# Kernel optimization log

Measured on AMD Instinct MI355X. Metric: run time of the kernel, lower is better.

## Reference

```python
import jax, jax.numpy as jnp
import numpy as np

D_MODEL = 1024
N_HEADS = 16
D_Q = 64
D_V = 64
N_SEG = 16
EPS_LN = 1e-5
EPS_MEM = 1e-6


def setup_inputs() -> dict:
    key = jax.random.key(0)
    ks = jax.random.split(key, 10)
    N, T = 4, 4096
    inp = {
        "query_sequences": jax.random.normal(ks[0], (N, T, D_MODEL), dtype=jnp.float32),
        "key_sequences": jax.random.normal(ks[1], (N, T, D_MODEL), dtype=jnp.float32),
        "value_sequences": jax.random.normal(ks[2], (N, T, D_MODEL), dtype=jnp.float32),
        "Wq": jax.random.normal(ks[3], (D_MODEL, N_HEADS * D_Q), dtype=jnp.float32) * 0.02,
        "Wk": jax.random.normal(ks[4], (D_MODEL, N_HEADS * D_Q), dtype=jnp.float32) * 0.02,
        "Wv": jax.random.normal(ks[5], (D_MODEL, N_HEADS * D_V), dtype=jnp.float32) * 0.02,
        "Wo": jax.random.normal(ks[6], (N_HEADS * D_V, D_MODEL), dtype=jnp.float32) * 0.02,
        "ln_w": jnp.ones((D_MODEL,), dtype=jnp.float32),
        "ln_b": jnp.zeros((D_MODEL,), dtype=jnp.float32),
        "beta": jnp.ones((1,), dtype=jnp.float32),
    }
    return inp


def _layer_norm(x, w, b):
    mu = jnp.mean(x, axis=-1, keepdims=True)
    var = jnp.var(x, axis=-1, keepdims=True)
    return (x - mu) * jax.lax.rsqrt(var + EPS_LN) * w + b


def reference(query_sequences, key_sequences, value_sequences, Wq, Wk, Wv, Wo, ln_w, ln_b, beta):
    N, t, _ = query_sequences.shape
    S = t // N_SEG  # segment length (256)

    # qkv_norm applied to q, and (self-attention) to k and v as well
    qn = _layer_norm(query_sequences, ln_w, ln_b)
    kn = _layer_norm(key_sequences, ln_w, ln_b)
    vn = _layer_norm(value_sequences, ln_w, ln_b)

    # project and split heads -> [N, H, t, d]
    qh = (qn @ Wq).reshape(N, t, N_HEADS, D_Q).transpose(0, 2, 1, 3)
    kh = (kn @ Wk).reshape(N, t, N_HEADS, D_Q).transpose(0, 2, 1, 3)
    vh = (vn @ Wv).reshape(N, t, N_HEADS, D_V).transpose(0, 2, 1, 3)

    # segment: [N_SEG, N, H, S, d] so lax.scan iterates segments sequentially
    seg = lambda x, d: x.reshape(N, N_HEADS, N_SEG, S, d).transpose(2, 0, 1, 3, 4)
    q_segs, k_segs, v_segs = seg(qh, D_Q), seg(kh, D_Q), seg(vh, D_V)

    b_gate = jax.nn.sigmoid(beta)[0]            # scalar mixing gate
    scale = 1.0 / np.sqrt(D_Q).astype(np.float32)
    causal = jnp.tril(jnp.ones((S, S), dtype=bool))

    def step(carry, xs):
        mem, z = carry                          # [N,H,Dq,Dv], [N,H,Dq]
        qs, ks_, vs = xs                        # [N,H,S,d]
        sq = jax.nn.elu(qs) + 1.0
        sk = jax.nn.elu(ks_) + 1.0
        # retrieve from compressive memory
        num = jnp.einsum('nhsd,nhde->nhse', sq, mem)
        den = jnp.einsum('nhsd,nhd->nhs', sq, z)[..., None] + EPS_MEM
        a_mem = num / den                       # [N,H,S,Dv]
        # local causal softmax attention within the segment
        scores = jnp.einsum('nhsd,nhtd->nhst', qs, ks_) * scale
        scores = jnp.where(causal, scores, -jnp.inf)
        probs = jax.nn.softmax(scores, axis=-1)
        attn = jnp.einsum('nhst,nhtd->nhsd', probs, vs)
        out = b_gate * a_mem + (1.0 - b_gate) * attn
        # linear memory update
        mem = mem + jnp.einsum('nhsd,nhse->nhde', sk, vs)
        z = z + sk.sum(axis=2)
        return (mem, z), out

    mem0 = jnp.zeros((N, N_HEADS, D_Q, D_V), dtype=query_sequences.dtype)
    z0 = jnp.zeros((N, N_HEADS, D_Q), dtype=query_sequences.dtype)
    _, outs = jax.lax.scan(step, (mem0, z0), (q_segs, k_segs, v_segs))

    # outs: [N_SEG, N, H, S, Dv] -> [N, t, H*Dv]
    seqs = outs.transpose(1, 0, 3, 2, 4).reshape(N, t, N_HEADS * D_V)
    return seqs @ Wo
```

## Files before the change

kernel.cpp:

```cpp
#include <hip/hip_runtime.h>
#include <stdint.h>
#include <math.h>


typedef __attribute__((ext_vector_type(8))) short bf16x8_t;
typedef __attribute__((ext_vector_type(4))) short short4_t;
typedef __attribute__((ext_vector_type(4))) float f32x4;

__device__ __forceinline__ float bf2f(short s){
  union { unsigned u; float f; } v; v.u = ((unsigned)(unsigned short)s) << 16; return v.f;
}
__device__ __forceinline__ short f2bf(float f){
  union { float fl; unsigned u; } v; v.fl = f;
  unsigned r = v.u + 0x7FFFu + ((v.u >> 16) & 1u);
  return (short)(unsigned short)(r >> 16);
}
__device__ __forceinline__ f32x4 mfma16(bf16x8_t a, bf16x8_t b, f32x4 c){
  return __builtin_amdgcn_mfma_f32_16x16x32_bf16(a, b, c, 0, 0, 0);
}
__device__ __forceinline__ void gl_lds16(const short* g, short* l){
  __builtin_amdgcn_global_load_lds((const __attribute__((address_space(1))) void*)g,
                                   (__attribute__((address_space(3))) void*)l, 16, 0, 0);
}

__global__ __launch_bounds__(256) void ln3(const float* __restrict__ xq, const float* __restrict__ xk,
                                           const float* __restrict__ xv,
                                           const float* __restrict__ gw, const float* __restrict__ gb,
                                           short* __restrict__ oq, short* __restrict__ ok,
                                           short* __restrict__ ov){
  const int row = blockIdx.x, which = blockIdx.y, tid = threadIdx.x;
  const float* x = which == 0 ? xq : which == 1 ? xk : xv;
  short* out     = which == 0 ? oq : which == 1 ? ok : ov;
  const float4 v = *reinterpret_cast<const float4*>(x + (size_t)row*1024 + tid*4);
  float s  = v.x + v.y + v.z + v.w;
  float s2 = v.x*v.x + v.y*v.y + v.z*v.z + v.w*v.w;
  #pragma unroll
  for (int off = 1; off < 64; off <<= 1){
    s  += __shfl_xor(s,  off);
    s2 += __shfl_xor(s2, off);
  }
  __shared__ float red[8];
  if ((tid & 63) == 0){ red[tid>>6] = s; red[4 + (tid>>6)] = s2; }
  __syncthreads();
  s  = red[0] + red[1] + red[2] + red[3];
  s2 = red[4] + red[5] + red[6] + red[7];
  const float mu  = s * (1.0f/1024.0f);
  const float var = s2 * (1.0f/1024.0f) - mu*mu;
  const float rs  = rsqrtf(var + 1e-5f);
  const float4 wv = *reinterpret_cast<const float4*>(gw + tid*4);
  const float4 bv = *reinterpret_cast<const float4*>(gb + tid*4);
  short4_t o;
  o[0] = f2bf((v.x-mu)*rs*wv.x + bv.x);
  o[1] = f2bf((v.y-mu)*rs*wv.y + bv.y);
  o[2] = f2bf((v.z-mu)*rs*wv.z + bv.z);
  o[3] = f2bf((v.w-mu)*rs*wv.w + bv.w);
  *reinterpret_cast<short4_t*>(out + (size_t)row*1024 + tid*4) = o;
}

__global__ __launch_bounds__(256) void wcast4(const float* __restrict__ W0, const float* __restrict__ W1,
                                              const float* __restrict__ W2, const float* __restrict__ W3,
                                              short* __restrict__ T0, short* __restrict__ T1,
                                              short* __restrict__ T2, short* __restrict__ T3){
  const int z = blockIdx.z;
  const float* W = z == 0 ? W0 : z == 1 ? W1 : z == 2 ? W2 : W3;
  short* Wt      = z == 0 ? T0 : z == 1 ? T1 : z == 2 ? T2 : T3;
  __shared__ float tile[64][65];
  const int bx = blockIdx.x, by = blockIdx.y, tid = threadIdx.x;
  #pragma unroll
  for (int p=0;p<4;++p){
    int idx = p*256 + tid;
    int r = idx >> 4, c4 = (idx & 15) << 2;
    const float4 v = *reinterpret_cast<const float4*>(W + (size_t)(by*64 + r)*1024 + bx*64 + c4);
    tile[r][c4+0] = v.x; tile[r][c4+1] = v.y; tile[r][c4+2] = v.z; tile[r][c4+3] = v.w;
  }
  __syncthreads();
  #pragma unroll
  for (int p=0;p<4;++p){
    int idx = p*256 + tid;
    int r = idx >> 4, c4 = (idx & 15) << 2;
    short4_t o;
    o[0] = f2bf(tile[c4+0][r]); o[1] = f2bf(tile[c4+1][r]);
    o[2] = f2bf(tile[c4+2][r]); o[3] = f2bf(tile[c4+3][r]);
    *reinterpret_cast<short4_t*>(Wt + (size_t)(bx*64 + r)*1024 + by*64 + c4) = o;
  }
}

__device__ __forceinline__ void remap_mc(int n, int& m0, int& c0){
  int xcd = n & 7, idx = n >> 3;
  m0 = ((xcd << 3) + (idx & 7)) << 8;
  c0 = (idx >> 3) << 8;
}

__device__ __forceinline__ void gemm_body(short* smem, const short* __restrict__ A,
                                          const short* __restrict__ Bt, void* __restrict__ C,
                                          int mode, int m0, int c0){
  short* As = smem;
  short* Bs = smem + 32768;
  const int tid = threadIdx.x;
  const int lane = tid & 63, wid = tid >> 6;
  const int wr = wid >> 2, wc = wid & 3;
  const int l15 = lane & 15, lhi = lane >> 4;

  const short* Asrc[4]; const short* Bsrc[4];
  #pragma unroll
  for (int p=0;p<4;++p){
    int i = tid + 512*p;
    int r = i >> 3, g = (i & 7) ^ (r & 7);
    Asrc[p] = A  + (size_t)(m0 + r)*1024 + g*8;
    Bsrc[p] = Bt + (size_t)(c0 + r)*1024 + g*8;
  }

  f32x4 acc[8][4];
  #pragma unroll
  for (int m=0;m<8;++m)
    #pragma unroll
    for (int n=0;n<4;++n) acc[m][n] = (f32x4){0.f,0.f,0.f,0.f};

  #define STAGE_A(t) { short* _d=&As[((t)&1)<<14]; int _k=(t)<<6; \
      gl_lds16(Asrc[0]+_k, _d+tid*8); gl_lds16(Asrc[1]+_k, _d+4096+tid*8); \
      gl_lds16(Asrc[2]+_k, _d+8192+tid*8); gl_lds16(Asrc[3]+_k, _d+12288+tid*8); }
  #define STAGE_B(t) { short* _d=&Bs[((t)&1)<<14]; int _k=(t)<<6; \
      gl_lds16(Bsrc[0]+_k, _d+tid*8); gl_lds16(Bsrc[1]+_k, _d+4096+tid*8); \
      gl_lds16(Bsrc[2]+_k, _d+8192+tid*8); gl_lds16(Bsrc[3]+_k, _d+12288+tid*8); }

  STAGE_A(0); STAGE_B(0);
  asm volatile("s_waitcnt vmcnt(0)" ::: "memory");
  __builtin_amdgcn_s_barrier();

  for (int t = 0; t < 16; ++t){
    const short* Ab = &As[(t & 1) << 14];
    const short* Bb = &Bs[(t & 1) << 14];
    if (t < 15){ STAGE_A(t+1); STAGE_B(t+1); }
    bf16x8_t af[4][2], bfr[4][2];
    #pragma unroll
    for (int m=0;m<4;++m){
      int r = wr*128 + m*16 + l15;
      #pragma unroll
      for (int ks=0;ks<2;++ks){
        int sl = (ks*4 + lhi) ^ (r & 7);
        af[m][ks] = *reinterpret_cast<const bf16x8_t*>(&Ab[r*64 + sl*8]);
      }
    }
    #pragma unroll
    for (int n=0;n<2;++n){
      int r = wc*64 + n*16 + l15;
      #pragma unroll
      for (int ks=0;ks<2;++ks){
        int sl = (ks*4 + lhi) ^ (r & 7);
        bfr[n][ks] = *reinterpret_cast<const bf16x8_t*>(&Bb[r*64 + sl*8]);
      }
    }
    __builtin_amdgcn_s_setprio(1);
    #pragma unroll
    for (int m=0;m<4;++m)
      #pragma unroll
      for (int n=0;n<2;++n)
        #pragma unroll
        for (int ks=0;ks<2;++ks)
          acc[m][n] = mfma16(af[m][ks], bfr[n][ks], acc[m][n]);
    __builtin_amdgcn_s_setprio(0);
    #pragma unroll
    for (int n=2;n<4;++n){
      int r = wc*64 + n*16 + l15;
      #pragma unroll
      for (int ks=0;ks<2;++ks){
        int sl = (ks*4 + lhi) ^ (r & 7);
        bfr[n][ks] = *reinterpret_cast<const bf16x8_t*>(&Bb[r*64 + sl*8]);
      }
    }
    __builtin_amdgcn_s_setprio(1);
    #pragma unroll
    for (int m=0;m<4;++m)
      #pragma unroll
      for (int n=2;n<4;++n)
        #pragma unroll
        for (int ks=0;ks<2;++ks)
          acc[m][n] = mfma16(af[m][ks], bfr[n][ks], acc[m][n]);
    __builtin_amdgcn_s_setprio(0);
    #pragma unroll
    for (int m=0;m<4;++m){
      int r = wr*128 + 64 + m*16 + l15;
      #pragma unroll
      for (int ks=0;ks<2;++ks){
        int sl = (ks*4 + lhi) ^ (r & 7);
        af[m][ks] = *reinterpret_cast<const bf16x8_t*>(&Ab[r*64 + sl*8]);
      }
    }
    __builtin_amdgcn_s_setprio(1);
    #pragma unroll
    for (int m=0;m<4;++m)
      #pragma unroll
      for (int n=0;n<2;++n)
        #pragma unroll
        for (int ks=0;ks<2;++ks)
          acc[4+m][n] = mfma16(af[m][ks], bfr[n][ks], acc[4+m][n]);
    __builtin_amdgcn_s_setprio(0);
    __builtin_amdgcn_s_setprio(1);
    #pragma unroll
    for (int m=0;m<4;++m)
      #pragma unroll
      for (int n=2;n<4;++n)
        #pragma unroll
        for (int ks=0;ks<2;++ks)
          acc[4+m][n] = mfma16(af[m][ks], bfr[n][ks], acc[4+m][n]);
    __builtin_amdgcn_s_setprio(0);
    asm volatile("s_waitcnt vmcnt(0)" ::: "memory");
    __builtin_amdgcn_s_barrier();
  }
  #undef STAGE_A
  #undef STAGE_B

  if (mode == 0){
    short* Cb = (short*)C;
    #pragma unroll
    for (int m=0;m<8;++m)
      #pragma unroll
      for (int n=0;n<4;++n)
        #pragma unroll
        for (int j=0;j<4;++j){
          int row = m0 + wr*128 + m*16 + lhi*4 + j;
          int col = c0 + wc*64 + n*16 + l15;
          size_t oidx = ((size_t)((row>>12)*16 + (col>>6)) * 4096 + (size_t)(row & 4095)) * 64 + (col & 63);
          Cb[oidx] = f2bf(acc[m][n][j]);
        }
  } else if (mode == 2){
    short* Cb = (short*)C;
    #pragma unroll
    for (int m=0;m<8;++m)
      #pragma unroll
      for (int n=0;n<4;++n){
        int rowb = m0 + wr*128 + m*16 + lhi*4;
        int col  = c0 + wc*64 + n*16 + l15;
        int nh = ((rowb>>12)<<4) + (col>>6);
        int e  = col & 63;
        int tt = rowb & 4095;
        short4_t o;
        #pragma unroll
        for (int j=0;j<4;++j) o[j] = f2bf(acc[m][n][j]);
        *reinterpret_cast<short4_t*>(&Cb[((size_t)nh*64 + e)*4096 + tt]) = o;
      }
  } else {
    float* Cf = (float*)C;
    #pragma unroll
    for (int m=0;m<8;++m)
      #pragma unroll
      for (int n=0;n<4;++n)
        #pragma unroll
        for (int j=0;j<4;++j){
          int row = m0 + wr*128 + m*16 + lhi*4 + j;
          int col = c0 + wc*64 + n*16 + l15;
          Cf[(size_t)row*1024 + col] = acc[m][n][j];
        }
  }
}

__global__ __launch_bounds__(512, 2) void gemm_qkv(const short* __restrict__ A0, const short* __restrict__ A1,
    const short* __restrict__ A2, const short* __restrict__ B0, const short* __restrict__ B1,
    const short* __restrict__ B2, short* __restrict__ C0, short* __restrict__ C1, short* __restrict__ C2){
  extern __shared__ short smem[];
  const int z = blockIdx.z;
  const short* A = z == 0 ? A0 : z == 1 ? A1 : A2;
  const short* B = z == 0 ? B0 : z == 1 ? B1 : B2;
  short* C       = z == 0 ? C0 : z == 1 ? C1 : C2;
  int m0, c0; remap_mc(blockIdx.x + 64*blockIdx.y, m0, c0);
  gemm_body(smem, A, B, (void*)C, z == 2 ? 2 : 0, m0, c0);
}

__global__ __launch_bounds__(512, 2) void gemm_wo(const short* __restrict__ A, const short* __restrict__ Bt,
                                                  float* __restrict__ C){
  extern __shared__ short smem[];
  int m0, c0; remap_mc(blockIdx.x + 64*blockIdx.y, m0, c0);
  gemm_body(smem, A, Bt, (void*)C, 1, m0, c0);
}

__global__ __launch_bounds__(256) void stageA(const short* __restrict__ kh, const short* __restrict__ vhT,
                                              short* __restrict__ delta_b, float* __restrict__ zd){
  const int seg = blockIdx.x, nh = blockIdx.y, tid = threadIdx.x;
  const int lane = tid & 63, w = tid >> 6;
  const int l15 = lane & 15, lhi = lane >> 4;
  __shared__ short skT[64*256];
  const size_t thead = (size_t)nh*4096 + (size_t)seg*256;

  #pragma unroll
  for (int ch=0; ch<8; ++ch){
    int s  = ch*32 + (tid>>3);
    int lc = (tid&7)*8;
    bf16x8_t kv = *reinterpret_cast<const bf16x8_t*>(kh + (thead + s)*64 + lc);
    #pragma unroll
    for (int j=0;j<8;++j){
      float f = bf2f(kv[j]);
      short sv = f2bf((f > 0.f) ? (f + 1.f) : __expf(f));
      int d = lc + j;
      int bo = ((d*256 + s) << 1) ^ (((d>>3)&7) << 4);
      *reinterpret_cast<short*>(reinterpret_cast<char*>(skT) + bo) = sv;
    }
  }
  __syncthreads();

  bf16x8_t ones;
  #pragma unroll
  for (int i=0;i<8;++i) ones[i] = (short)0x3F80;

  f32x4 dacc[4], zacc[4];
  #pragma unroll
  for (int jf=0;jf<4;++jf){ dacc[jf] = (f32x4){0.f,0.f,0.f,0.f}; zacc[jf] = (f32x4){0.f,0.f,0.f,0.f}; }

  #pragma unroll
  for (int ks=0; ks<8; ++ks){
    bf16x8_t av = *reinterpret_cast<const bf16x8_t*>(
        vhT + ((size_t)nh*64 + w*16 + l15)*4096 + (size_t)seg*256 + ks*32 + lhi*8);
    #pragma unroll
    for (int jf=0;jf<4;++jf){
      int d  = jf*16 + l15;
      int so = ks*32 + lhi*8;
      int bo = ((d*256 + so) << 1) ^ (((d>>3)&7) << 4);
      bf16x8_t bk = *reinterpret_cast<const bf16x8_t*>(reinterpret_cast<char*>(skT) + bo);
      dacc[jf] = mfma16(av, bk, dacc[jf]);
      if (w == 0) zacc[jf] = mfma16(ones, bk, zacc[jf]);
    }
  }

  short* dp = delta_b + (size_t)(seg*64 + nh)*4096;
  #pragma unroll
  for (int jf=0;jf<4;++jf)
    #pragma unroll
    for (int j=0;j<4;++j)
      dp[(w*16 + lhi*4 + j)*64 + jf*16 + l15] = f2bf(dacc[jf][j]);
  if (w == 0 && lhi == 0){
    #pragma unroll
    for (int jf=0;jf<4;++jf)
      zd[(size_t)(seg*64 + nh)*64 + jf*16 + l15] = zacc[jf][0];
  }
}

__global__ __launch_bounds__(256) void stageB(const short* __restrict__ delta_b, const float* __restrict__ zd,
                                              short* __restrict__ mpre_b, float* __restrict__ zpre){
  const int c = blockIdx.x, nh = blockIdx.y, tid = threadIdx.x;
  const int idx = c*256 + tid;
  float acc = 0.f;
  for (int seg=0; seg<16; ++seg){
    size_t b = (size_t)(seg*64 + nh)*4096 + idx;
    mpre_b[b] = f2bf(acc);
    acc += bf2f(delta_b[b]);
  }
  if (c == 0 && tid < 64){
    float za = 0.f;
    for (int seg=0; seg<16; ++seg){
      size_t zb = (size_t)(seg*64 + nh)*64 + tid;
      zpre[zb] = za;
      za += zd[zb];
    }
  }
}

__global__ __launch_bounds__(256, 3) void stageC(const short* __restrict__ qh, const short* __restrict__ kh,
    const short* __restrict__ vhT, const short* __restrict__ mpre_b, const float* __restrict__ z_pre,
    const float* __restrict__ beta, short* __restrict__ seqs)
{
  const int seg  = blockIdx.x;
  const int nh   = blockIdx.y;
  const int tid = threadIdx.x;
  const int lane = tid & 63, w = tid >> 6;
  const int l15 = lane & 15, lhi = lane >> 4;

  __shared__ float zl[64];
  __shared__ short pl[4][32][72];

  const size_t thead = (size_t)nh*4096 + (size_t)seg*256;

  if (tid < 64) zl[tid] = z_pre[(size_t)(seg*64 + nh)*64 + tid];
  __syncthreads();

  const float bg = 1.f / (1.f + __expf(-beta[0]));
  const float scale = 0.125f;
  bf16x8_t ones;
  #pragma unroll
  for (int i=0;i<8;++i) ones[i] = (short)0x3F80;
  const short* mpbase = mpre_b + (size_t)(seg*64 + nh)*4096;
  const int nb = nh >> 4, hh = nh & 15;

  for (int p = 0; p < 2; ++p){
    const int tile = p ? (7 - w) : w;
    const int nkt  = (tile >> 1) + 1;
    const int rb   = tile * 32;

    bf16x8_t aq[2][2];
    #pragma unroll
    for (int m=0;m<2;++m)
      #pragma unroll
      for (int ks=0;ks<2;++ks)
        aq[m][ks] = *reinterpret_cast<const bf16x8_t*>(qh + (thead + rb + m*16 + l15)*64 + ks*32 + lhi*8);

    f32x4 o_acc[2][4], l_acc[2];
    #pragma unroll
    for (int m=0;m<2;++m){
      l_acc[m] = (f32x4){0.f,0.f,0.f,0.f};
      #pragma unroll
      for (int jf=0;jf<4;++jf) o_acc[m][jf] = (f32x4){0.f,0.f,0.f,0.f};
    }

    for (int kt = 0; kt < nkt; ++kt){
      bf16x8_t bv[4][2];
      #pragma unroll
      for (int jf=0;jf<4;++jf)
        #pragma unroll
        for (int ks2=0;ks2<2;++ks2)
          bv[jf][ks2] = *reinterpret_cast<const bf16x8_t*>(
              vhT + ((size_t)nh*64 + jf*16 + l15)*4096 + (size_t)seg*256 + kt*64 + ks2*32 + lhi*8);

      f32x4 s_acc[2][4];
      #pragma unroll
      for (int m=0;m<2;++m)
        #pragma unroll
        for (int jf=0;jf<4;++jf) s_acc[m][jf] = (f32x4){0.f,0.f,0.f,0.f};
      #pragma unroll
      for (int ks=0;ks<2;++ks){
        bf16x8_t bk[4];
        #pragma unroll
        for (int jf=0;jf<4;++jf)
          bk[jf] = *reinterpret_cast<const bf16x8_t*>(kh + (thead + kt*64 + jf*16 + l15)*64 + ks*32 + lhi*8);
        #pragma unroll
        for (int m=0;m<2;++m)
          #pragma unroll
          for (int jf=0;jf<4;++jf)
            s_acc[m][jf] = mfma16(aq[m][ks], bk[jf], s_acc[m][jf]);
      }
      const bool lastkt = (kt == nkt - 1);
      #pragma unroll
      for (int m=0;m<2;++m)
        #pragma unroll
        for (int jf=0;jf<4;++jf)
          #pragma unroll
          for (int j=0;j<4;++j){
            float vv = s_acc[m][jf][j] * scale;
            if (lastkt){
              int sr = rb + m*16 + lhi*4 + j;
              int tc = kt*64 + jf*16 + l15;
              if (tc > sr) vv = -INFINITY;
            }
            float pv = __expf(vv);
            pl[w][m*16 + lhi*4 + j][jf*16 + l15] = f2bf(pv);
          }
      #pragma unroll
      for (int ks2=0;ks2<2;++ks2){
        bf16x8_t ap[2];
        #pragma unroll
        for (int m=0;m<2;++m)
          ap[m] = *reinterpret_cast<const bf16x8_t*>(&pl[w][m*16 + l15][ks2*32 + lhi*8]);
        #pragma unroll
        for (int m=0;m<2;++m){
          l_acc[m] = mfma16(ap[m], ones, l_acc[m]);
          #pragma unroll
          for (int jf=0;jf<4;++jf)
            o_acc[m][jf] = mfma16(ap[m], bv[jf][ks2], o_acc[m][jf]);
        }
      }
    }

    bf16x8_t sq[2][2];
    #pragma unroll
    for (int m=0;m<2;++m)
      #pragma unroll
      for (int ks=0;ks<2;++ks)
        #pragma unroll
        for (int i=0;i<8;++i){
          float f = bf2f(aq[m][ks][i]);
          sq[m][ks][i] = f2bf((f > 0.f) ? (f + 1.f) : __expf(f));
        }
    bf16x8_t bz[2];
    #pragma unroll
    for (int ks=0;ks<2;++ks)
      #pragma unroll
      for (int i=0;i<8;++i) bz[ks][i] = f2bf(zl[ks*32 + lhi*8 + i]);

    f32x4 n_acc[2][4], d_acc[2];
    #pragma unroll
    for (int m=0;m<2;++m){
      d_acc[m] = (f32x4){0.f,0.f,0.f,0.f};
      #pragma unroll
      for (int jf=0;jf<4;++jf) n_acc[m][jf] = (f32x4){0.f,0.f,0.f,0.f};
    }
    #pragma unroll
    for (int ks=0;ks<2;++ks){
      bf16x8_t bm[4];
      #pragma unroll
      for (int jf=0;jf<4;++jf)
        bm[jf] = *reinterpret_cast<const bf16x8_t*>(mpbase + (jf*16 + l15)*64 + ks*32 + lhi*8);
      #pragma unroll
      for (int m=0;m<2;++m){
        #pragma unroll
        for (int jf=0;jf<4;++jf) n_acc[m][jf] = mfma16(sq[m][ks], bm[jf], n_acc[m][jf]);
        d_acc[m] = mfma16(sq[m][ks], bz[ks], d_acc[m]);
      }
    }

    #pragma unroll
    for (int m=0;m<2;++m)
      #pragma unroll
      for (int jf=0;jf<4;++jf)
        #pragma unroll
        for (int j=0;j<4;++j){
          float attn = o_acc[m][jf][j] / l_acc[m][j];
          float amem = n_acc[m][jf][j] / (d_acc[m][j] + 1e-6f);
          float ov = bg*amem + (1.f-bg)*attn;
          int srow = rb + m*16 + lhi*4 + j;
          seqs[((size_t)nb*4096 + (size_t)seg*256 + srow)*1024 + hh*64 + jf*16 + l15] = f2bf(ov);
        }
  }
}

extern "C" void kernel_launch(void* const* d_in, const int* in_sizes, int n_in,
                              void* d_out, int out_size, void* d_ws, size_t ws_size,
                              hipStream_t stream){
  (void)in_sizes; (void)n_in; (void)out_size; (void)ws_size;
  const float* q    = (const float*)d_in[0];
  const float* k    = (const float*)d_in[1];
  const float* v    = (const float*)d_in[2];
  const float* Wq   = (const float*)d_in[3];
  const float* Wk   = (const float*)d_in[4];
  const float* Wv   = (const float*)d_in[5];
  const float* Wo   = (const float*)d_in[6];
  const float* lnw  = (const float*)d_in[7];
  const float* lnb  = (const float*)d_in[8];
  const float* beta = (const float*)d_in[9];
  char* ws = (char*)d_ws;
  const size_t MB = 1024ull*1024ull;
  short* WqT    = (short*)(ws + 0*MB);
  short* WkT    = (short*)(ws + 2*MB);
  short* WvT    = (short*)(ws + 4*MB);
  short* WoT    = (short*)(ws + 6*MB);
  short* xn_v   = (short*)(ws + 8*MB);
  short* seqs   = xn_v;
  short* qh     = (short*)(ws + 40*MB);
  short* kh     = (short*)(ws + 72*MB);
  short* vhT    = (short*)(ws + 104*MB);
  short* delta_b= (short*)(ws + 136*MB);
  float* zd     = (float*)(ws + 144*MB);
  short* mpre_b = (short*)(ws + 145*MB);
  float* zpre   = (float*)(ws + 153*MB);
  short* xn_q   = (short*)d_out;
  short* xn_k   = (short*)d_out + 16384ull*1024ull;

  wcast4<<<dim3(16,16,4),256,0,stream>>>(Wq,Wk,Wv,Wo, WqT,WkT,WvT,WoT);
  ln3<<<dim3(16384,3),256,0,stream>>>(q,k,v, lnw,lnb, xn_q,xn_k,xn_v);

  const size_t lds_gemm = 131072;
  gemm_qkv<<<dim3(64,4,3),512,lds_gemm,stream>>>(xn_q,xn_k,xn_v, WqT,WkT,WvT, qh,kh,vhT);

  stageA<<<dim3(16,64),256,0,stream>>>(kh, vhT, delta_b, zd);
  stageB<<<dim3(16,64),256,0,stream>>>(delta_b, zd, mpre_b, zpre);
  stageC<<<dim3(16,64),256,0,stream>>>(qh, kh, vhT, mpre_b, zpre, beta, seqs);
  gemm_wo<<<dim3(64,4),512,lds_gemm,stream>>>(seqs, WoT, (float*)d_out);
}
```

Baseline: 314.9 us.

## Stage K/V tiles in LDS with double-buffering and give each wave 64 query rows

StageC now cooperatively loads 64-row K and V tiles into XOR-swizzled shared memory with global_load_lds, double-buffered across the four key tiles. Each wave now owns one 64-row query block instead of two 32-row tiles. Before, every wave re-read K and V from global memory on its own. The load-balancing pairing of tiles (w and 7-w) is gone, so waves do uneven causal work (1 to 4 key tiles), and there are more per-iteration barriers. Register use rises (4x4 accumulators) and the occupancy hint is dropped.

```diff
diff --git a/kernel.cpp b/kernel.cpp
--- a/kernel.cpp
+++ b/kernel.cpp
@@ -353,7 +353,7 @@
   }
 }
 
-__global__ __launch_bounds__(256, 3) void stageC(const short* __restrict__ qh, const short* __restrict__ kh,
+__global__ __launch_bounds__(256) void stageC(const short* __restrict__ qh, const short* __restrict__ kh,
     const short* __restrict__ vhT, const short* __restrict__ mpre_b, const float* __restrict__ z_pre,
     const float* __restrict__ beta, short* __restrict__ seqs)
 {
@@ -363,12 +363,37 @@
   const int lane = tid & 63, w = tid >> 6;
   const int l15 = lane & 15, lhi = lane >> 4;
 
+  __shared__ short Ks[2][4096];
+  __shared__ short Vs[2][4096];
   __shared__ float zl[64];
-  __shared__ short pl[4][32][72];
+  __shared__ short pl[4][64][72];
 
   const size_t thead = (size_t)nh*4096 + (size_t)seg*256;
 
+  const short* Ksrc[2]; const short* Vsrc[2];
+  #pragma unroll
+  for (int p=0;p<2;++p){
+    int i = tid + 256*p, r = i >> 3, g = (i & 7) ^ (r & 7);
+    Ksrc[p] = kh + (thead + r)*64 + g*8;
+    Vsrc[p] = vhT + ((size_t)nh*64 + r)*4096 + (size_t)seg*256 + g*8;
+  }
+  #define STAGE_KV(kt) { short* _kd = Ks[(kt)&1]; short* _vd = Vs[(kt)&1]; \
+      gl_lds16(Ksrc[0] + (kt)*4096, _kd + tid*8); \
+      gl_lds16(Ksrc[1] + (kt)*4096, _kd + 2048 + tid*8); \
+      gl_lds16(Vsrc[0] + (kt)*64,  _vd + tid*8); \
+      gl_lds16(Vsrc[1] + (kt)*64,  _vd + 2048 + tid*8); }
+
   if (tid < 64) zl[tid] = z_pre[(size_t)(seg*64 + nh)*64 + tid];
+
+  bf16x8_t aq[4][2];
+  #pragma unroll
+  for (int m=0;m<4;++m)
+    #pragma unroll
+    for (int ks=0;ks<2;++ks)
+      aq[m][ks] = *reinterpret_cast<const bf16x8_t*>(qh + (thead + w*64 + m*16 + l15)*64 + ks*32 + lhi*8);
+
+  STAGE_KV(0);
+  asm volatile("s_waitcnt vmcnt(0)" ::: "memory");
   __syncthreads();
 
   const float bg = 1.f / (1.f + __expf(-beta[0]));
@@ -376,66 +401,51 @@
   bf16x8_t ones;
   #pragma unroll
   for (int i=0;i<8;++i) ones[i] = (short)0x3F80;
-  const short* mpbase = mpre_b + (size_t)(seg*64 + nh)*4096;
-  const int nb = nh >> 4, hh = nh & 15;
-
-  for (int p = 0; p < 2; ++p){
-    const int tile = p ? (7 - w) : w;
-    const int nkt  = (tile >> 1) + 1;
-    const int rb   = tile * 32;
-
-    bf16x8_t aq[2][2];
-    #pragma unroll
-    for (int m=0;m<2;++m)
-      #pragma unroll
-      for (int ks=0;ks<2;++ks)
-        aq[m][ks] = *reinterpret_cast<const bf16x8_t*>(qh + (thead + rb + m*16 + l15)*64 + ks*32 + lhi*8);
-
-    f32x4 o_acc[2][4], l_acc[2];
-    #pragma unroll
-    for (int m=0;m<2;++m){
-      l_acc[m] = (f32x4){0.f,0.f,0.f,0.f};
-      #pragma unroll
-      for (int jf=0;jf<4;++jf) o_acc[m][jf] = (f32x4){0.f,0.f,0.f,0.f};
-    }
-
-    for (int kt = 0; kt < nkt; ++kt){
-      bf16x8_t bv[4][2];
-      #pragma unroll
-      for (int jf=0;jf<4;++jf)
-        #pragma unroll
-        for (int ks2=0;ks2<2;++ks2)
-          bv[jf][ks2] = *reinterpret_cast<const bf16x8_t*>(
-              vhT + ((size_t)nh*64 + jf*16 + l15)*4096 + (size_t)seg*256 + kt*64 + ks2*32 + lhi*8);
-
-      f32x4 s_acc[2][4];
-      #pragma unroll
-      for (int m=0;m<2;++m)
+
+  f32x4 o_acc[4][4], l_acc[4];
+  #pragma unroll
+  for (int m=0;m<4;++m){
+    l_acc[m] = (f32x4){0.f,0.f,0.f,0.f};
+    #pragma unroll
+    for (int jf=0;jf<4;++jf) o_acc[m][jf] = (f32x4){0.f,0.f,0.f,0.f};
+  }
+
+  for (int kt = 0; kt < 4; ++kt){
+    const short* Kb = Ks[kt & 1];
+    const short* Vb = Vs[kt & 1];
+    if (kt < 3) STAGE_KV(kt+1);
+    if (kt <= w){
+      f32x4 s_acc[4][4];
+      #pragma unroll
+      for (int m=0;m<4;++m)
         #pragma unroll
         for (int jf=0;jf<4;++jf) s_acc[m][jf] = (f32x4){0.f,0.f,0.f,0.f};
       #pragma unroll
       for (int ks=0;ks<2;++ks){
         bf16x8_t bk[4];
         #pragma unroll
-        for (int jf=0;jf<4;++jf)
-          bk[jf] = *reinterpret_cast<const bf16x8_t*>(kh + (thead + kt*64 + jf*16 + l15)*64 + ks*32 + lhi*8);
-        #pragma unroll
-        for (int m=0;m<2;++m)
+        for (int jf=0;jf<4;++jf){
+          int r = jf*16 + l15;
+          int sl = (ks*4 + lhi) ^ (r & 7);
+          bk[jf] = *reinterpret_cast<const bf16x8_t*>(&Kb[r*64 + sl*8]);
+        }
+        #pragma unroll
+        for (int m=0;m<4;++m)
           #pragma unroll
           for (int jf=0;jf<4;++jf)
             s_acc[m][jf] = mfma16(aq[m][ks], bk[jf], s_acc[m][jf]);
       }
-      const bool lastkt = (kt == nkt - 1);
-      #pragma unroll
-      for (int m=0;m<2;++m)
+      const bool diag = (kt == w);
+      #pragma unroll
+      for (int m=0;m<4;++m)
         #pragma unroll
         for (int jf=0;jf<4;++jf)
           #pragma unroll
           for (int j=0;j<4;++j){
             float vv = s_acc[m][jf][j] * scale;
-            if (lastkt){
-              int sr = rb + m*16 + lhi*4 + j;
-              int tc = kt*64 + jf*16 + l15;
+            if (diag){
+              int sr = (w<<6) + m*16 + lhi*4 + j;
+              int tc = (kt<<6) + jf*16 + l15;
               if (tc > sr) vv = -INFINITY;
             }
             float pv = __expf(vv);
@@ -443,70 +453,83 @@
           }
       #pragma unroll
       for (int ks2=0;ks2<2;++ks2){
-        bf16x8_t ap[2];
-        #pragma unroll
-        for (int m=0;m<2;++m)
+        bf16x8_t ap[4], bv[4];
+        #pragma unroll
+        for (int m=0;m<4;++m)
           ap[m] = *reinterpret_cast<const bf16x8_t*>(&pl[w][m*16 + l15][ks2*32 + lhi*8]);
         #pragma unroll
-        for (int m=0;m<2;++m){
+        for (int jf=0;jf<4;++jf){
+          int e = jf*16 + l15;
+          int sl = (ks2*4 + lhi) ^ (e & 7);
+          bv[jf] = *reinterpret_cast<const bf16x8_t*>(&Vb[e*64 + sl*8]);
+        }
+        #pragma unroll
+        for (int m=0;m<4;++m){
           l_acc[m] = mfma16(ap[m], ones, l_acc[m]);
           #pragma unroll
           for (int jf=0;jf<4;++jf)
-            o_acc[m][jf] = mfma16(ap[m], bv[jf][ks2], o_acc[m][jf]);
+            o_acc[m][jf] = mfma16(ap[m], bv[jf], o_acc[m][jf]);
         }
       }
     }
-
-    bf16x8_t sq[2][2];
-    #pragma unroll
-    for (int m=0;m<2;++m)
-      #pragma unroll
-      for (int ks=0;ks<2;++ks)
-        #pragma unroll
-        for (int i=0;i<8;++i){
-          float f = bf2f(aq[m][ks][i]);
-          sq[m][ks][i] = f2bf((f > 0.f) ? (f + 1.f) : __expf(f));
-        }
-    bf16x8_t bz[2];
+    if (kt < 3){
+      asm volatile("s_waitcnt vmcnt(0)" ::: "memory");
+      __builtin_amdgcn_s_barrier();
+    }
+  }
+  #undef STAGE_KV
+
+  bf16x8_t sq[4][2];
+  #pragma unroll
+  for (int m=0;m<4;++m)
     #pragma unroll
     for (int ks=0;ks<2;++ks)
       #pragma unroll
-      for (int i=0;i<8;++i) bz[ks][i] = f2bf(zl[ks*32 + lhi*8 + i]);
-
-    f32x4 n_acc[2][4], d_acc[2];
-    #pragma unroll
-    for (int m=0;m<2;++m){
-      d_acc[m] = (f32x4){0.f,0.f,0.f,0.f};
-      #pragma unroll
-      for (int jf=0;jf<4;++jf) n_acc[m][jf] = (f32x4){0.f,0.f,0.f,0.f};
-    }
-    #pragma unroll
-    for (int ks=0;ks<2;++ks){
-      bf16x8_t bm[4];
-      #pragma unroll
-      for (int jf=0;jf<4;++jf)
-        bm[jf] = *reinterpret_cast<const bf16x8_t*>(mpbase + (jf*16 + l15)*64 + ks*32 + lhi*8);
-      #pragma unroll
-      for (int m=0;m<2;++m){
-        #pragma unroll
-        for (int jf=0;jf<4;++jf) n_acc[m][jf] = mfma16(sq[m][ks], bm[jf], n_acc[m][jf]);
-        d_acc[m] = mfma16(sq[m][ks], bz[ks], d_acc[m]);
-      }
-    }
-
-    #pragma unroll
-    for (int m=0;m<2;++m)
-      #pragma unroll
-      for (int jf=0;jf<4;++jf)
-        #pragma unroll
-        for (int j=0;j<4;++j){
-          float attn = o_acc[m][jf][j] / l_acc[m][j];
-          float amem = n_acc[m][jf][j] / (d_acc[m][j] + 1e-6f);
-          float ov = bg*amem + (1.f-bg)*attn;
-          int srow = rb + m*16 + lhi*4 + j;
-          seqs[((size_t)nb*4096 + (size_t)seg*256 + srow)*1024 + hh*64 + jf*16 + l15] = f2bf(ov);
-        }
-  }
+      for (int i=0;i<8;++i){
+        float f = bf2f(aq[m][ks][i]);
+        sq[m][ks][i] = f2bf((f > 0.f) ? (f + 1.f) : __expf(f));
+      }
+  bf16x8_t bz[2];
+  #pragma unroll
+  for (int ks=0;ks<2;++ks)
+    #pragma unroll
+    for (int i=0;i<8;++i) bz[ks][i] = f2bf(zl[ks*32 + lhi*8 + i]);
+
+  const short* mpbase = mpre_b + (size_t)(seg*64 + nh)*4096;
+  f32x4 n_acc[4][4], d_acc[4];
+  #pragma unroll
+  for (int m=0;m<4;++m){
+    d_acc[m] = (f32x4){0.f,0.f,0.f,0.f};
+    #pragma unroll
+    for (int jf=0;jf<4;++jf) n_acc[m][jf] = (f32x4){0.f,0.f,0.f,0.f};
+  }
+  #pragma unroll
+  for (int ks=0;ks<2;++ks){
+    bf16x8_t bm[4];
+    #pragma unroll
+    for (int jf=0;jf<4;++jf)
+      bm[jf] = *reinterpret_cast<const bf16x8_t*>(mpbase + (jf*16 + l15)*64 + ks*32 + lhi*8);
+    #pragma unroll
+    for (int m=0;m<4;++m){
+      #pragma unroll
+      for (int jf=0;jf<4;++jf) n_acc[m][jf] = mfma16(sq[m][ks], bm[jf], n_acc[m][jf]);
+      d_acc[m] = mfma16(sq[m][ks], bz[ks], d_acc[m]);
+    }
+  }
+
+  const int nb = nh >> 4, hh = nh & 15;
+  #pragma unroll
+  for (int m=0;m<4;++m)
+    #pragma unroll
+    for (int jf=0;jf<4;++jf)
+      #pragma unroll
+      for (int j=0;j<4;++j){
+        float attn = o_acc[m][jf][j] / l_acc[m][j];
+        float amem = n_acc[m][jf][j] / (d_acc[m][j] + 1e-6f);
+        float ov = bg*amem + (1.f-bg)*attn;
+        int srow = (w<<6) + m*16 + lhi*4 + j;
+        seqs[((size_t)nb*4096 + (size_t)seg*256 + srow)*1024 + hh*64 + jf*16 + l15] = f2bf(ov);
+      }
 }
 
 extern "C" void kernel_launch(void* const* d_in, const int* in_sizes, int n_in,
```

New measurement: 310.4 us. About the same (-1.4%).
